# Kernel optimization log

Hardware: AMD Instinct MI355X
Metric: run time of the kernel (lower is better)

## Reference

```python
import jax, jax.numpy as jnp
import numpy as np

N = 50000       # nodes
E = 800000      # directed edges
F_IN = 128      # input feature dim
HID = 128       # hidden channels
DEPTH = 3


def glorot(key, shape):
    lim = (6.0 / (shape[0] + shape[-1])) ** 0.5
    return jax.random.uniform(key, shape, jnp.float32, -lim, lim)


def setup_inputs():
    key = jax.random.key(0)
    ks = jax.random.split(key, 20)
    inp = {
        "x": jax.random.normal(ks[0], (N, F_IN), jnp.float32),
        "edge_index": jax.random.randint(ks[1], (E, 2), 0, N),
        "y": jax.random.randint(ks[2], (N,), 0, 2),
    }
    dd = [(F_IN, HID), (HID, HID), (HID, HID), (HID, HID)]
    for i, (a, b) in enumerate(dd):
        inp[f"Wd{i}"] = glorot(ks[3 + i], (a, b))
        inp[f"bd{i}"] = jnp.zeros((b,), jnp.float32)
    for i in range(DEPTH):
        inp[f"Wp{i}"] = glorot(ks[7 + i], (2 * HID,))
        inp[f"bp{i}"] = jnp.zeros((), jnp.float32)
    du = [(2 * HID, HID), (2 * HID, HID), (2 * HID + F_IN, 1)]
    for i, (a, b) in enumerate(du):
        inp[f"Wu{i}"] = glorot(ks[10 + i], (a, b))
        inp[f"bu{i}"] = jnp.zeros((b,), jnp.float32)
    return inp


def gcn_conv(x, src, dst, ew, W, b):
    """GCNConv(improved=True): A_hat = A + 2I, symmetric normalization.
    ew masks invalid (deduped/padded) edges with 0."""
    n = x.shape[0]
    deg = 2.0 + jax.ops.segment_sum(ew, dst, num_segments=n)  # self-loop weight 2
    dinv = jax.lax.rsqrt(deg)
    xw = x @ W                                   # [n, out]
    norm = ew * dinv[src] * dinv[dst]            # [E]
    out = jax.ops.segment_sum(xw[src] * norm[:, None], dst, num_segments=n)
    out = out + (2.0 * dinv * dinv)[:, None] * xw  # self-loop contribution
    return out + b


def connected_components(src, dst, sel, n):
    """Weak CC over selected edges via min-label propagation + pointer jumping.
    Returns per-node label = min node index in its component."""
    s = jnp.where(sel, src, 0)  # masked edges become (0,0) self-loops
    d = jnp.where(sel, dst, 0)

    def body(state):
        lab, _ = state
        m = jnp.minimum(lab[s], lab[d])
        new = lab.at[s].min(m).at[d].min(m)
        new = new[new]
        new = new[new]
        return new, jnp.any(new != lab)

    lab, _ = jax.lax.while_loop(lambda st: st[1], body,
                                (jnp.arange(n), jnp.array(True)))
    return lab


def cluster_pool(x, src, dst, ew, Wp, bp):
    """ClusterPooling (eval mode): score edges, contract score>0.5 edges,
    merge components (sum of members scaled by mean intra-cluster edge score).
    Pooled graph keeps N slots; cluster ids are representative node indices."""
    n, hid = x.shape
    valid = (ew > 0) & (src != dst)
    s = jax.nn.sigmoid(x[src] @ Wp[:hid] + x[dst] @ Wp[hid:] + bp)  # [E]
    sel = valid & (s > 0.5)
    cluster = jax.lax.stop_gradient(connected_components(src, dst, sel, n))
    csrc = cluster[src]
    ssum = jax.ops.segment_sum(jnp.where(sel, s, 0.0), csrc, num_segments=n)
    scnt = jax.ops.segment_sum(sel.astype(x.dtype), csrc, num_segments=n)
    w = jnp.where(scnt > 0, ssum / jnp.maximum(scnt, 1.0), 1.0)  # singletons -> 1
    new_x = jax.ops.segment_sum(x, cluster, num_segments=n) * w[:, None]
    # remap edges to clusters, drop self-loops, coalesce duplicates (static shape)
    a = jnp.where(valid, cluster[src], n)
    b = jnp.where(valid, cluster[dst], n)
    loop = a == b
    a = jnp.where(loop, n, a)
    b = jnp.where(loop, n, b)
    order = jnp.lexsort((b, a))
    a, b = a[order], b[order]
    dup = jnp.concatenate([jnp.zeros((1,), bool),
                           (a[1:] == a[:-1]) & (b[1:] == b[:-1])])
    keep = (a < n) & (~dup)
    new_ew = keep.astype(x.dtype)
    a = jnp.where(keep, a, 0)
    b = jnp.where(keep, b, 0)
    return new_x, a, b, new_ew, (src, dst, ew, cluster)


def reference(x, edge_index, y,
              Wd0, bd0, Wd1, bd1, Wd2, bd2, Wd3, bd3,
              Wp0, bp0, Wp1, bp1, Wp2, bp2,
              Wu0, bu0, Wu1, bu1, Wu2, bu2):
    Wd = [Wd0, Wd1, Wd2, Wd3]; bd = [bd0, bd1, bd2, bd3]
    Wp = [Wp0, Wp1, Wp2]; bp = [bp0, bp1, bp2]
    Wu = [Wu0, Wu1, Wu2]; bu = [bu0, bu1, bu2]
    src = edge_index[:, 0]
    dst = edge_index[:, 1]
    ew = jnp.ones(src.shape[0], x.dtype)
    x_in = x
    memory, infos = [], []
    for i in range(DEPTH):
        x = jax.nn.relu(gcn_conv(x, src, dst, ew, Wd[i], bd[i]))
        memory.append(x)
        x, src, dst, ew, info = cluster_pool(x, src, dst, ew, Wp[i], bp[i])
        infos.append(info)
    memory[0] = jnp.concatenate([memory[0], x_in], axis=-1)
    x = gcn_conv(x, src, dst, ew, Wd[3], bd[3])
    for i in range(DEPTH):
        src, dst, ew, cluster = infos.pop()
        x = x[cluster]                                  # unpool
        x = jnp.concatenate([memory.pop(), x], axis=-1)  # skip connection
        x = gcn_conv(x, src, dst, ew, Wu[i], bu[i])
        if i < DEPTH - 1:
            x = jax.nn.relu(x)
    return jax.nn.sigmoid(x).ravel()
```

## Files before the change

kernel.cpp:

```cpp
#include <hip/hip_runtime.h>
#include <math.h>

#define NN 50000
#define EE 800000
#define HID 128
#define HSZ (1u<<21)
#define CC_ROUNDS 8
#define GN 196
#define WH 512


static __device__ __forceinline__ float sigmoid_ref(float t) {
  if (t >= 0.f) { float e = expf(-t); return 1.f / (1.f + e); }
  float e = expf(t); return e / (1.f + e);
}

static __device__ __forceinline__ int edge_count(const int* cntp, int cnst) {
  return cntp ? *cntp : cnst;
}


__global__ void k_split_edges(const int* __restrict__ ei, int* __restrict__ s, int* __restrict__ d) {
  int T = gridDim.x*blockDim.x;
  for (int e = blockIdx.x*blockDim.x+threadIdx.x; e < EE; e += T) {
    s[e] = ei[2*e]; d[e] = ei[2*e+1];
  }
}

__global__ void k_degree(const int* __restrict__ eB, const int* cntp, int cnst, int* __restrict__ deg) {
  int n = edge_count(cntp, cnst);
  int T = gridDim.x*blockDim.x;
  for (int e = blockIdx.x*blockDim.x+threadIdx.x; e < n; e += T)
    atomicAdd(&deg[eB[e]], 1);
}

__global__ void k_scan1(const int* __restrict__ deg, int* __restrict__ rp, int* __restrict__ bsum) {
  __shared__ int sh[256];
  int tid = threadIdx.x; int i = blockIdx.x*256 + tid;
  int v = (i < NN) ? deg[i] : 0;
  sh[tid] = v; __syncthreads();
  for (int off = 1; off < 256; off <<= 1) {
    int t = (tid >= off) ? sh[tid-off] : 0;
    __syncthreads(); sh[tid] += t; __syncthreads();
  }
  if (i < NN) rp[i] = sh[tid] - v;
  if (tid == 255) bsum[blockIdx.x] = sh[255];
}

__global__ void k_scan2(int* __restrict__ bsum, int* __restrict__ rp, int nb) {
  __shared__ int sh[256];
  int tid = threadIdx.x;
  int v = (tid < nb) ? bsum[tid] : 0;
  sh[tid] = v; __syncthreads();
  for (int off = 1; off < 256; off <<= 1) {
    int t = (tid >= off) ? sh[tid-off] : 0;
    __syncthreads(); sh[tid] += t; __syncthreads();
  }
  if (tid < nb) bsum[tid] = sh[tid] - v;
  if (tid == 255) rp[NN] = sh[255];
}

__global__ void k_scan3(int* __restrict__ rp, const int* __restrict__ bsum, int* __restrict__ cursor,
                        const int* __restrict__ deg, float* __restrict__ dinv) {
  int i = blockIdx.x*256 + threadIdx.x;
  if (i < NN) {
    int r = rp[i] + bsum[blockIdx.x];
    rp[i] = r; cursor[i] = r;
    if (dinv) dinv[i] = (float)(1.0 / sqrt((double)(deg[i] + 2)));
  }
}

__global__ void k_csrfill(const int* __restrict__ eA, const int* __restrict__ eB,
                          const int* cntp, int cnst,
                          int* __restrict__ cursor, int* __restrict__ csr, int* __restrict__ dstE) {
  int n = edge_count(cntp, cnst);
  int T = gridDim.x*blockDim.x;
  for (int e = blockIdx.x*blockDim.x+threadIdx.x; e < n; e += T) {
    int d = eB[e];
    int p = atomicAdd(&cursor[d], 1);
    csr[p] = eA[e];
    dstE[p] = d;
  }
}


__global__ __launch_bounds__(256) void k_matmul(
    const float* __restrict__ A0, const int* __restrict__ idx0,
    const float* __restrict__ A1, const int* __restrict__ idx1,
    int K, const float* __restrict__ W, const float* __restrict__ dinv,
    float* __restrict__ C)
{
  __shared__ __align__(16) float As[64][68];
  __shared__ __align__(16) float Bs[64][HID];
  const int tid  = threadIdx.x;
  const int row0 = blockIdx.x * 64;
  const int colg = (tid & 31) * 4;
  const int rowg = (tid >> 5) * 8;
  float acc[8][4];
  #pragma unroll
  for (int i = 0; i < 8; ++i) { acc[i][0]=0.f; acc[i][1]=0.f; acc[i][2]=0.f; acc[i][3]=0.f; }

  for (int kc = 0; kc < K; kc += 64) {
    const float* Asrc = (kc < 128) ? A0 : A1;
    const int*   aidx = (kc < 128) ? idx0 : idx1;
    const int klocal  = (kc < 128) ? kc : (kc - 128);
    #pragma unroll
    for (int t = tid; t < 64*16; t += 256) {
      int r  = t >> 4;
      int k4 = (t & 15) << 2;
      int grow = row0 + r;
      if (grow >= NN) grow = NN - 1;
      int gr = aidx ? aidx[grow] : grow;
      float4 v = *(const float4*)(Asrc + (size_t)gr*HID + klocal + k4);
      As[k4+0][r] = v.x; As[k4+1][r] = v.y; As[k4+2][r] = v.z; As[k4+3][r] = v.w;
    }
    #pragma unroll
    for (int t = tid; t < 64*32; t += 256) {
      int kk = t >> 5;
      int c4 = (t & 31) << 2;
      *(float4*)&Bs[kk][c4] = *(const float4*)(W + (size_t)(kc+kk)*HID + c4);
    }
    __syncthreads();
    #pragma unroll 8
    for (int k = 0; k < 64; ++k) {
      float4 a0 = *(const float4*)&As[k][rowg];
      float4 a1 = *(const float4*)&As[k][rowg+4];
      float4 b  = *(const float4*)&Bs[k][colg];
      float ar[8] = {a0.x,a0.y,a0.z,a0.w,a1.x,a1.y,a1.z,a1.w};
      #pragma unroll
      for (int i = 0; i < 8; ++i) {
        acc[i][0] += ar[i]*b.x; acc[i][1] += ar[i]*b.y;
        acc[i][2] += ar[i]*b.z; acc[i][3] += ar[i]*b.w;
      }
    }
    __syncthreads();
  }
  #pragma unroll
  for (int i = 0; i < 8; ++i) {
    int r = row0 + rowg + i;
    if (r < NN) {
      float dv = dinv[r];
      *(float4*)(C + (size_t)r*HID + colg) =
        make_float4(acc[i][0]*dv, acc[i][1]*dv, acc[i][2]*dv, acc[i][3]*dv);
    }
  }
}

__global__ __launch_bounds__(256) void k_convinit(
    const float* __restrict__ xs, const float* __restrict__ dinv,
    const float* __restrict__ bias, float* __restrict__ out)
{
  int T = gridDim.x*blockDim.x;
  const float4* x4 = (const float4*)xs;
  float4* o4 = (float4*)out;
  const float4* b4 = (const float4*)bias;
  for (int i = blockIdx.x*blockDim.x+threadIdx.x; i < NN*HID/4; i += T) {
    int v = i >> 5;
    float c = 2.f*dinv[v];
    float4 xv = x4[i];
    float4 bb = b4[i & 31];
    o4[i] = make_float4(xv.x*c+bb.x, xv.y*c+bb.y, xv.z*c+bb.z, xv.w*c+bb.w);
  }
}

__global__ __launch_bounds__(256) void k_edgeagg(
    const float* __restrict__ xs, const int* __restrict__ csr, const int* __restrict__ dstE,
    const float* __restrict__ dinv, float* __restrict__ out,
    const int* cntp, int cnst)
{
  int n = edge_count(cntp, cnst);
  const int lane = threadIdx.x & 31;
  const int grp  = (blockIdx.x*blockDim.x + threadIdx.x) >> 5;
  const int ngrp = (gridDim.x*blockDim.x) >> 5;
  int chunk = (n + ngrp - 1) / ngrp;
  int p0 = grp*chunk;
  int p1 = p0 + chunk; if (p1 > n) p1 = n;
  if (p0 >= p1) return;

  int cur = dstE[p0];
  float4 acc = make_float4(0.f,0.f,0.f,0.f);
  int s = csr[p0];
  float4 xv = *(const float4*)(xs + (size_t)s*HID + lane*4);
  for (int p = p0; p < p1; ++p) {
    int pn = p + 1;
    int d = dstE[p];
    float4 xn = make_float4(0.f,0.f,0.f,0.f);
    int sn = 0;
    if (pn < p1) { sn = csr[pn]; xn = *(const float4*)(xs + (size_t)sn*HID + lane*4); }
    if (d != cur) {
      float dv = dinv[cur];
      float* o = out + (size_t)cur*HID + lane*4;
      atomicAdd(o+0, acc.x*dv); atomicAdd(o+1, acc.y*dv);
      atomicAdd(o+2, acc.z*dv); atomicAdd(o+3, acc.w*dv);
      acc = make_float4(0.f,0.f,0.f,0.f);
      cur = d;
    }
    acc.x += xv.x; acc.y += xv.y; acc.z += xv.z; acc.w += xv.w;
    xv = xn;
  }
  float dv = dinv[cur];
  float* o = out + (size_t)cur*HID + lane*4;
  atomicAdd(o+0, acc.x*dv); atomicAdd(o+1, acc.y*dv);
  atomicAdd(o+2, acc.z*dv); atomicAdd(o+3, acc.w*dv);
}

__global__ void k_relu(float* __restrict__ x, int n4) {
  int T = gridDim.x*blockDim.x;
  float4* x4 = (float4*)x;
  for (int i = blockIdx.x*blockDim.x+threadIdx.x; i < n4; i += T) {
    float4 v = x4[i];
    v.x = fmaxf(v.x,0.f); v.y = fmaxf(v.y,0.f); v.z = fmaxf(v.z,0.f); v.w = fmaxf(v.w,0.f);
    x4[i] = v;
  }
}


__global__ __launch_bounds__(256) void k_node_ab(
    const float* __restrict__ h, const float* __restrict__ Wp,
    float* __restrict__ an, float* __restrict__ bn)
{
  int l = threadIdx.x & 63;
  int sub = threadIdx.x >> 6;
  float w0 = Wp[l], w1 = Wp[64+l], w2 = Wp[128+l], w3 = Wp[192+l];
  for (int g = blockIdx.x; g*4 < NN; g += gridDim.x) {
    int v = g*4 + sub;
    if (v >= NN) continue;
    float h0 = h[(size_t)v*HID + l];
    float h1 = h[(size_t)v*HID + 64 + l];
    float a = h0*w0 + h1*w1;
    float b = h0*w2 + h1*w3;
    #pragma unroll
    for (int off = 32; off; off >>= 1) { a += __shfl_down(a, off); b += __shfl_down(b, off); }
    if (l == 0) { an[v] = a; bn[v] = b; }
  }
}

__global__ void k_labinit(int* __restrict__ lab, int* __restrict__ flags,
                          int* __restrict__ selcnt, int* ecnt_next,
                          float* __restrict__ ssum2) {
  int i = blockIdx.x*256 + threadIdx.x;
  int T = gridDim.x*256;
  if (i < NN) lab[i] = i;
  for (int j = i; j < 2*NN; j += T) ssum2[j] = 0.f;
  if (i < 32) flags[i] = 0;
  if (i == 32) *selcnt = 0;
  if (i == 33 && ecnt_next) *ecnt_next = 0;
}

__global__ __launch_bounds__(256) void k_score_sel(
    const int* __restrict__ eA, const int* __restrict__ eB, const int* cntp, int cnst,
    const float* __restrict__ an, const float* __restrict__ bn, const float* __restrict__ bp,
    int* __restrict__ selA, int* __restrict__ selB, float* __restrict__ selS,
    int* __restrict__ selcnt)
{
  int n = edge_count(cntp, cnst);
  int T = gridDim.x*blockDim.x;
  int lane = threadIdx.x & 63;
  for (int e = blockIdx.x*blockDim.x+threadIdx.x; e < n; e += T) {
    int a = eA[e], b = eB[e];
    bool pred = false; float s = 0.f;
    if (a != b) {
      s = sigmoid_ref(an[a] + bn[b] + bp[0]);
      pred = s > 0.5f;
    }
    unsigned long long mask = __ballot(pred);
    if (mask) {
      int leader = __ffsll((long long)mask) - 1;
      int total  = __popcll(mask);
      int base = 0;
      if (lane == leader) base = atomicAdd(selcnt, total);
      base = __shfl(base, leader);
      if (pred) {
        int off = __popcll(mask & ((1ull << lane) - 1));
        selA[base+off] = a; selB[base+off] = b; selS[base+off] = s;
      }
    }
  }
}

__global__ __launch_bounds__(256) void k_hook(
    const int* __restrict__ selA, const int* __restrict__ selB, const int* __restrict__ selcnt,
    int* __restrict__ lab, const int* flagPrev, int* __restrict__ flagCur)
{
  if (flagPrev && *flagPrev == 0) return;
  int n = *selcnt;
  int T = gridDim.x*blockDim.x;
  bool changed = false;
  for (int i = blockIdx.x*blockDim.x+threadIdx.x; i < n; i += T) {
    int a = selA[i], b = selB[i];
    int la = lab[a], lb = lab[b];
    if (la == lb) continue;
    int pla = lab[la], plb = lab[lb];
    int m = min(pla, plb);
    if (la > m && lab[a] > m) atomicMin(&lab[a], m);
    if (lb > m && lab[b] > m) atomicMin(&lab[b], m);
    if (pla > m) atomicMin(&lab[la], m);
    if (plb > m) atomicMin(&lab[lb], m);
    changed = true;
  }
  unsigned long long m2 = __ballot(changed);
  if (m2 && (threadIdx.x & 63) == __ffsll((long long)m2) - 1) *flagCur = 1;
}

__global__ void k_jump(int* __restrict__ lab, const int* flagPrev, int* __restrict__ flagCur) {
  if (flagPrev && *flagPrev == 0) return;
  int i = blockIdx.x*256 + threadIdx.x;
  bool changed = false;
  if (i < NN) {
    int l0 = lab[i];
    int l = lab[l0]; l = lab[l]; l = lab[l];
    if (l < l0) { lab[i] = l; changed = true; }
  }
  unsigned long long m2 = __ballot(changed);
  if (m2 && (threadIdx.x & 63) == __ffsll((long long)m2) - 1) *flagCur = 1;
}

__global__ __launch_bounds__(256) void k_wsum(
    const int* __restrict__ selA, const float* __restrict__ selS,
    const int* __restrict__ selcnt, const int* __restrict__ cl,
    float* __restrict__ ssum, float* __restrict__ scnt)
{
  __shared__ int key[WH];
  __shared__ float vs[WH];
  __shared__ float vc[WH];
  int n = *selcnt;
  for (int i = threadIdx.x; i < WH; i += 256) { key[i] = -1; vs[i] = 0.f; vc[i] = 0.f; }
  __syncthreads();
  int T = gridDim.x*blockDim.x;
  for (int e = blockIdx.x*blockDim.x+threadIdx.x; e < n; e += T) {
    int c = cl[selA[e]];
    float s = selS[e];
    unsigned h = ((unsigned)c * 2654435761u) & (WH-1);
    bool done = false;
    for (int probe = 0; probe < 32; ++probe) {
      int k = key[h];
      if (k == c) { atomicAdd(&vs[h], s); atomicAdd(&vc[h], 1.f); done = true; break; }
      if (k == -1) {
        int old = atomicCAS(&key[h], -1, c);
        if (old == -1 || old == c) { atomicAdd(&vs[h], s); atomicAdd(&vc[h], 1.f); done = true; break; }
      }
      h = (h+1) & (WH-1);
    }
    if (!done) { atomicAdd(&ssum[c], s); atomicAdd(&scnt[c], 1.f); }
  }
  __syncthreads();
  for (int i = threadIdx.x; i < WH; i += 256) {
    if (key[i] >= 0) { atomicAdd(&ssum[key[i]], vs[i]); atomicAdd(&scnt[key[i]], vc[i]); }
  }
}

__global__ __launch_bounds__(128) void k_poolsum(const float* __restrict__ h,
                                                 const int* __restrict__ cl, float* __restrict__ p) {
  int f = threadIdx.x;
  int base = blockIdx.x * 64;
  int cur = -1; float acc = 0.f;
  for (int j = 0; j < 64; ++j) {
    int v = base + j;
    if (v >= NN) break;
    int c = cl[v];
    float x = h[(size_t)v*HID + f];
    if (c == cur) acc += x;
    else {
      if (cur >= 0) atomicAdd(&p[(size_t)cur*HID + f], acc);
      cur = c; acc = x;
    }
  }
  if (cur >= 0) atomicAdd(&p[(size_t)cur*HID + f], acc);
}

__global__ void k_poolscale(float* __restrict__ p, const float* __restrict__ ssum,
                            const float* __restrict__ scnt) {
  int T = gridDim.x*blockDim.x;
  float4* p4 = (float4*)p;
  for (int i = blockIdx.x*blockDim.x+threadIdx.x; i < NN*HID/4; i += T) {
    int r = i >> 5;
    float c = scnt[r];
    float w = (c > 0.f) ? ssum[r]/c : 1.f;
    float4 v = p4[i];
    v.x *= w; v.y *= w; v.z *= w; v.w *= w;
    p4[i] = v;
  }
}

__global__ __launch_bounds__(256) void k_contract(
    const int* __restrict__ eA, const int* __restrict__ eB, const int* cntp, int cnst,
    const int* __restrict__ cl, unsigned long long* __restrict__ tab,
    int* __restrict__ outA, int* __restrict__ outB, int* __restrict__ ocnt, int lev)
{
  int n = edge_count(cntp, cnst);
  int T = gridDim.x*blockDim.x;
  int lane = threadIdx.x & 63;
  for (int e = blockIdx.x*blockDim.x+threadIdx.x; e < n; e += T) {
    int s = eA[e], d = eB[e];
    bool keep = false; int a = 0, b = 0;
    if (s != d) {
      a = cl[s]; b = cl[d];
      if (a != b) {
        unsigned long long key = ((unsigned long long)lev << 34) |
                                 ((unsigned long long)a << 17) | (unsigned long long)b;
        unsigned long long hh = key * 0x9E3779B97F4A7C15ull;
        unsigned idx = (unsigned)(hh >> 40) & (HSZ - 1);
        while (true) {
          unsigned long long prev = atomicCAS(&tab[idx], ~0ull, key);
          if (prev == ~0ull) { keep = true; break; }
          if (prev == key) break;
          idx = (idx + 1) & (HSZ - 1);
        }
      }
    }
    unsigned long long mask = __ballot(keep);
    if (mask) {
      int leader = __ffsll((long long)mask) - 1;
      int total  = __popcll(mask);
      int base = 0;
      if (lane == leader) base = atomicAdd(ocnt, total);
      base = __shfl(base, leader);
      if (keep) {
        int off = __popcll(mask & ((1ull << lane) - 1));
        outA[base+off] = a; outB[base+off] = b;
      }
    }
  }
}


__global__ __launch_bounds__(256) void k_matvec384(
    const float* __restrict__ h1, const float* __restrict__ xin,
    const float* __restrict__ u1, const int* __restrict__ cl0,
    const float* __restrict__ Wu2, float* __restrict__ zw)
{
  int l = threadIdx.x & 63;
  int sub = threadIdx.x >> 6;
  float w0 = Wu2[l],     w1 = Wu2[64+l],  w2 = Wu2[128+l];
  float w3 = Wu2[192+l], w4 = Wu2[256+l], w5 = Wu2[320+l];
  for (int g = blockIdx.x; g*4 < NN; g += gridDim.x) {
    int v = g*4 + sub;
    if (v >= NN) continue;
    int gg = cl0[v];
    float s = h1[(size_t)v*HID + l]       * w0
            + h1[(size_t)v*HID + 64 + l]  * w1
            + xin[(size_t)v*HID + l]      * w2
            + xin[(size_t)v*HID + 64 + l] * w3
            + u1[(size_t)gg*HID + l]      * w4
            + u1[(size_t)gg*HID + 64 + l] * w5;
    #pragma unroll
    for (int off = 32; off; off >>= 1) s += __shfl_down(s, off);
    if (l == 0) zw[v] = s;
  }
}

__global__ void k_final(const float* __restrict__ zw, const int* __restrict__ rp,
                        const int* __restrict__ csr, const float* __restrict__ dinv,
                        const float* __restrict__ bu, float* __restrict__ out) {
  int T = gridDim.x*blockDim.x;
  for (int v = blockIdx.x*blockDim.x+threadIdx.x; v < NN; v += T) {
    float acc = 0.f;
    int p0 = rp[v], p1 = rp[v+1];
    for (int p = p0; p < p1; ++p) { int s = csr[p]; acc += zw[s]*dinv[s]; }
    float dv = dinv[v];
    float t = acc*dv + 2.f*dv*dv*zw[v] + bu[0];
    out[v] = sigmoid_ref(t);
  }
}


extern "C" void kernel_launch(void* const* d_in, const int* in_sizes, int n_in,
                              void* d_out, int out_size, void* d_ws, size_t ws_size,
                              hipStream_t stream) {
  const float* x_in = (const float*)d_in[0];
  const int*   ei   = (const int*)d_in[1];
  const float* Wd0 = (const float*)d_in[3];  const float* bd0 = (const float*)d_in[4];
  const float* Wd1 = (const float*)d_in[5];  const float* bd1 = (const float*)d_in[6];
  const float* Wd2 = (const float*)d_in[7];  const float* bd2 = (const float*)d_in[8];
  const float* Wd3 = (const float*)d_in[9];  const float* bd3 = (const float*)d_in[10];
  const float* Wp0 = (const float*)d_in[11]; const float* bp0 = (const float*)d_in[12];
  const float* Wp1 = (const float*)d_in[13]; const float* bp1 = (const float*)d_in[14];
  const float* Wp2 = (const float*)d_in[15]; const float* bp2 = (const float*)d_in[16];
  const float* Wu0 = (const float*)d_in[17]; const float* bu0 = (const float*)d_in[18];
  const float* Wu1 = (const float*)d_in[19]; const float* bu1 = (const float*)d_in[20];
  const float* Wu2 = (const float*)d_in[21]; const float* bu2 = (const float*)d_in[22];
  float* out = (float*)d_out;
  (void)in_sizes; (void)n_in; (void)out_size;

  char* wp = (char*)d_ws;
  auto alloc = [&](size_t bytes) -> void* {
    void* p = (void*)wp;
    wp += (bytes + 255) & ~(size_t)255;
    return p;
  };
  float* B[6]; for (int i = 0; i < 6; ++i) B[i] = (float*)alloc((size_t)NN*HID*4);
  int *eA[4], *eB[4];
  for (int i = 0; i < 4; ++i) { eA[i] = (int*)alloc((size_t)EE*4); eB[i] = (int*)alloc((size_t)EE*4); }
  int* cl[3];      for (int i = 0; i < 3; ++i) cl[i]    = (int*)alloc((size_t)NN*4);
  float* dinvL[4]; for (int i = 0; i < 4; ++i) dinvL[i] = (float*)alloc((size_t)NN*4);
  int* rpL[4]; int* csrL[4]; int* dstL[4];
  for (int i = 0; i < 4; ++i) {
    rpL[i]  = (int*)alloc((size_t)(NN+1)*4);
    csrL[i] = (int*)alloc((size_t)EE*4);
    dstL[i] = (int*)alloc((size_t)EE*4);
  }
  int*   selA = (int*)alloc((size_t)EE*4);
  int*   selB = (int*)alloc((size_t)EE*4);
  float* selS = (float*)alloc((size_t)EE*4);
  int* deg    = (int*)alloc((size_t)NN*4);
  int* cursor = (int*)alloc((size_t)NN*4);
  int* bsum   = (int*)alloc(256*4);
  float* an   = (float*)alloc((size_t)NN*4);
  float* bn   = (float*)alloc((size_t)NN*4);
  float* ssum = (float*)alloc((size_t)2*NN*4);
  float* scnt = ssum + NN;
  float* zw   = (float*)alloc((size_t)NN*4);
  int* selcnt = (int*)alloc(256);
  int* ecnt   = (int*)alloc(256);
  int* flags  = (int*)alloc(256);
  unsigned long long* tab = (unsigned long long*)alloc((size_t)HSZ*8);
  if ((size_t)(wp - (char*)d_ws) > ws_size) return;

  k_split_edges<<<1024,256,0,stream>>>(ei, eA[0], eB[0]);
  hipMemsetAsync(tab, 0xFF, (size_t)HSZ*8, stream);

  auto cntp = [&](int lev) -> const int* { return lev ? (ecnt + lev) : nullptr; };

  auto build_level = [&](int lev) {
    hipMemsetAsync(deg, 0, (size_t)NN*4, stream);
    k_degree<<<512,256,0,stream>>>(eB[lev], cntp(lev), EE, deg);
    k_scan1<<<GN,256,0,stream>>>(deg, rpL[lev], bsum);
    k_scan2<<<1,256,0,stream>>>(bsum, rpL[lev], GN);
    k_scan3<<<GN,256,0,stream>>>(rpL[lev], bsum, cursor, deg, dinvL[lev]);
    k_csrfill<<<512,256,0,stream>>>(eA[lev], eB[lev], cntp(lev), EE, cursor, csrL[lev], dstL[lev]);
  };

  auto do_conv = [&](const float* A0, const int* i0, const float* A1, const int* i1, int K,
                     const float* W, const float* bias, int lev, float* xs, float* outp, int relu) {
    k_matmul<<<(NN+63)/64,256,0,stream>>>(A0, i0, A1, i1, K, W, dinvL[lev], xs);
    k_convinit<<<512,256,0,stream>>>(xs, dinvL[lev], bias, outp);
    k_edgeagg<<<1024,256,0,stream>>>(xs, csrL[lev], dstL[lev], dinvL[lev], outp, cntp(lev), EE);
    if (relu) k_relu<<<512,256,0,stream>>>(outp, NN*HID/4);
  };

  auto do_pool = [&](const float* h, int lev, int ci, float* p, const float* Wp, const float* bp) {
    k_node_ab<<<512,256,0,stream>>>(h, Wp, an, bn);
    k_labinit<<<GN,256,0,stream>>>(cl[ci], flags, selcnt, ecnt + lev + 1, ssum);
    k_score_sel<<<512,256,0,stream>>>(eA[lev], eB[lev], cntp(lev), EE, an, bn, bp,
                                      selA, selB, selS, selcnt);
    for (int r = 0; r < CC_ROUNDS; ++r) {
      const int* fp = r ? (flags + r - 1) : nullptr;
      k_hook<<<512,256,0,stream>>>(selA, selB, selcnt, cl[ci], fp, flags + r);
      k_jump<<<GN,256,0,stream>>>(cl[ci], fp, flags + r);
    }
    k_wsum<<<64,256,0,stream>>>(selA, selS, selcnt, cl[ci], ssum, scnt);
    hipMemsetAsync(p, 0, (size_t)NN*HID*4, stream);
    k_poolsum<<<(NN+63)/64,128,0,stream>>>(h, cl[ci], p);
    k_poolscale<<<1024,256,0,stream>>>(p, ssum, scnt);
    k_contract<<<512,256,0,stream>>>(eA[lev], eB[lev], cntp(lev), EE, cl[ci], tab,
                                     eA[lev+1], eB[lev+1], ecnt + lev + 1, lev);
  };

  build_level(0);
  do_conv(x_in, nullptr, nullptr, nullptr, 128, Wd0, bd0, 0, B[5], B[0], 1);
  do_pool(B[0], 0, 0, B[3], Wp0, bp0);
  build_level(1);
  do_conv(B[3], nullptr, nullptr, nullptr, 128, Wd1, bd1, 1, B[5], B[1], 1);
  do_pool(B[1], 1, 1, B[3], Wp1, bp1);
  build_level(2);
  do_conv(B[3], nullptr, nullptr, nullptr, 128, Wd2, bd2, 2, B[5], B[2], 1);
  do_pool(B[2], 2, 2, B[3], Wp2, bp2);
  build_level(3);
  do_conv(B[3], nullptr, nullptr, nullptr, 128, Wd3, bd3, 3, B[5], B[4], 0);
  do_conv(B[2], nullptr, B[4], cl[2], 256, Wu0, bu0, 2, B[5], B[3], 1);
  do_conv(B[1], nullptr, B[3], cl[1], 256, Wu1, bu1, 1, B[5], B[4], 1);
  k_matvec384<<<512,256,0,stream>>>(B[0], x_in, B[4], cl[0], Wu2, zw);
  k_final<<<512,256,0,stream>>>(zw, rpL[0], csrL[0], dinvL[0], bu2, out);
}
```

Baseline: 1.909 ms.

## Restructure edge aggregation with fixed chunks, shared-memory indices, deeper prefetch, plain interior stores

The edge aggregation kernel now gives each 32-lane group a fixed chunk of 128 sorted edges instead of a grid-stride-derived chunk, and stages the source and destination indices in shared memory. It keeps four feature rows in flight as a software prefetch ring. Destination segments that lie wholly inside a chunk are written with plain float4 read-modify-write instead of four atomics, since no other group touches them. Only the first and last segment of each chunk still use atomics. The grid grows to cover all edges at one chunk per group, which adds launch parallelism but also more boundary atomics.

```diff
diff --git a/kernel.cpp b/kernel.cpp
--- a/kernel.cpp
+++ b/kernel.cpp
@@ -8,6 +8,7 @@
 #define CC_ROUNDS 8
 #define GN 196
 #define WH 512
+#define CH 128
 
 
 static __device__ __forceinline__ float sigmoid_ref(float t) {
@@ -168,35 +169,59 @@
     const float* __restrict__ dinv, float* __restrict__ out,
     const int* cntp, int cnst)
 {
+  __shared__ int sh_s[8][CH];
+  __shared__ int sh_d[8][CH];
   int n = edge_count(cntp, cnst);
   const int lane = threadIdx.x & 31;
-  const int grp  = (blockIdx.x*blockDim.x + threadIdx.x) >> 5;
-  const int ngrp = (gridDim.x*blockDim.x) >> 5;
-  int chunk = (n + ngrp - 1) / ngrp;
-  int p0 = grp*chunk;
-  int p1 = p0 + chunk; if (p1 > n) p1 = n;
-  if (p0 >= p1) return;
-
-  int cur = dstE[p0];
+  const int gsub = threadIdx.x >> 5;
+  const int grp  = blockIdx.x*8 + gsub;
+  const int p0   = grp * CH;
+  if (p0 >= n) return;
+  const int cnt = min(CH, n - p0);
+
+  for (int j = lane; j < cnt; j += 32) {
+    sh_s[gsub][j] = csr[p0 + j];
+    sh_d[gsub][j] = dstE[p0 + j];
+  }
+
+  float4 pf[4];
+  #pragma unroll
+  for (int j = 0; j < 4; ++j) {
+    if (j < cnt) {
+      int s = sh_s[gsub][j];
+      pf[j] = *(const float4*)(xs + (size_t)s*HID + lane*4);
+    }
+  }
+
+  int cur = sh_d[gsub][0];
   float4 acc = make_float4(0.f,0.f,0.f,0.f);
-  int s = csr[p0];
-  float4 xv = *(const float4*)(xs + (size_t)s*HID + lane*4);
-  for (int p = p0; p < p1; ++p) {
-    int pn = p + 1;
-    int d = dstE[p];
-    float4 xn = make_float4(0.f,0.f,0.f,0.f);
-    int sn = 0;
-    if (pn < p1) { sn = csr[pn]; xn = *(const float4*)(xs + (size_t)sn*HID + lane*4); }
+  int flushes = 0;
+
+  #pragma unroll 4
+  for (int i = 0; i < cnt; ++i) {
+    float4 xv = pf[i & 3];
+    int jn = i + 4;
+    if (jn < cnt) {
+      int sn = sh_s[gsub][jn];
+      pf[i & 3] = *(const float4*)(xs + (size_t)sn*HID + lane*4);
+    }
+    int d = sh_d[gsub][i];
     if (d != cur) {
       float dv = dinv[cur];
       float* o = out + (size_t)cur*HID + lane*4;
-      atomicAdd(o+0, acc.x*dv); atomicAdd(o+1, acc.y*dv);
-      atomicAdd(o+2, acc.z*dv); atomicAdd(o+3, acc.w*dv);
+      if (flushes == 0) {
+        atomicAdd(o+0, acc.x*dv); atomicAdd(o+1, acc.y*dv);
+        atomicAdd(o+2, acc.z*dv); atomicAdd(o+3, acc.w*dv);
+      } else {
+        float4 ov = *(float4*)o;
+        ov.x += acc.x*dv; ov.y += acc.y*dv; ov.z += acc.z*dv; ov.w += acc.w*dv;
+        *(float4*)o = ov;
+      }
+      ++flushes;
       acc = make_float4(0.f,0.f,0.f,0.f);
       cur = d;
     }
     acc.x += xv.x; acc.y += xv.y; acc.z += xv.z; acc.w += xv.w;
-    xv = xn;
   }
   float dv = dinv[cur];
   float* o = out + (size_t)cur*HID + lane*4;
@@ -530,11 +555,12 @@
     k_csrfill<<<512,256,0,stream>>>(eA[lev], eB[lev], cntp(lev), EE, cursor, csrL[lev], dstL[lev]);
   };
 
+  const int GAGG = (EE + 8*CH - 1) / (8*CH);
   auto do_conv = [&](const float* A0, const int* i0, const float* A1, const int* i1, int K,
                      const float* W, const float* bias, int lev, float* xs, float* outp, int relu) {
     k_matmul<<<(NN+63)/64,256,0,stream>>>(A0, i0, A1, i1, K, W, dinvL[lev], xs);
     k_convinit<<<512,256,0,stream>>>(xs, dinvL[lev], bias, outp);
-    k_edgeagg<<<1024,256,0,stream>>>(xs, csrL[lev], dstL[lev], dinvL[lev], outp, cntp(lev), EE);
+    k_edgeagg<<<GAGG,256,0,stream>>>(xs, csrL[lev], dstL[lev], dinvL[lev], outp, cntp(lev), EE);
     if (relu) k_relu<<<512,256,0,stream>>>(outp, NN*HID/4);
   };
 
```

Result: faster. 1.725 ms (-9.6%).
